# Optimization experiments

Hardware: AMD Instinct MI355X
Metric: run time of the kernel (lower is better)

Reference implementation:

```python
import jax, jax.numpy as jnp
import numpy as np

N_NODES = 100000
N_EDGES = 1200000
FEAT = 64
AVG_D_LOG = float(np.log(13.0))  # log(avg_degree + 1), avg_degree = 12
EPS_STD = 1e-5   # PNA std epsilon
EPS_BN = 1e-5    # torch BatchNorm1d default eps


def setup_inputs() -> dict:
    key = jax.random.key(0)
    k_h, k_norm, k_src, k_dst = jax.random.split(key, 4)
    h = jax.random.normal(k_h, (N_NODES, FEAT), dtype=jnp.float32)
    norm = jax.random.uniform(k_norm, (N_NODES, 1), dtype=jnp.float32)
    e = jnp.zeros((N_EDGES, 1), dtype=jnp.float32)  # unused by the layer
    src = jax.random.randint(k_src, (N_EDGES,), 0, N_NODES, dtype=jnp.int32)
    dst = jnp.sort(jax.random.randint(k_dst, (N_EDGES,), 0, N_NODES, dtype=jnp.int32))
    bn_weight = jnp.ones((FEAT,), dtype=jnp.float32)
    bn_bias = jnp.zeros((FEAT,), dtype=jnp.float32)
    return {"h": h, "norm": norm, "e": e, "bn_weight": bn_weight,
            "bn_bias": bn_bias, "src": src, "dst": dst}


def reference(h, norm, e, bn_weight, bn_bias, src, dst):
    N, F = h.shape
    hn = h * norm                           # [N, F] pre-scaled node features
    m = hn[src]                             # [E, F] gathered messages (copy_u)

    ones = jnp.ones_like(dst, dtype=hn.dtype)
    deg = jax.ops.segment_sum(ones, dst, num_segments=N, indices_are_sorted=True)  # [N]
    deg_safe = jnp.maximum(deg, 1.0)
    has_nb = (deg > 0)[:, None]             # zero in-degree nodes get zeros (DGL)

    s1 = jax.ops.segment_sum(m, dst, num_segments=N, indices_are_sorted=True)
    s2 = jax.ops.segment_sum(m * m, dst, num_segments=N, indices_are_sorted=True)
    mean = s1 / deg_safe[:, None]
    var = jax.nn.relu(s2 / deg_safe[:, None] - mean * mean)
    std = jnp.sqrt(var + EPS_STD)
    mx = jnp.where(has_nb, jax.ops.segment_max(m, dst, num_segments=N, indices_are_sorted=True), 0.0)
    mn = jnp.where(has_nb, jax.ops.segment_min(m, dst, num_segments=N, indices_are_sorted=True), 0.0)

    agg = jnp.concatenate([mean, mx, mn, std], axis=1)          # [N, 4F]

    logD = jnp.log(deg + 1.0)[:, None]                           # [N, 1]
    amp = agg * (logD / AVG_D_LOG)                               # amplification scaler
    att = agg * (AVG_D_LOG / jnp.where(logD > 0, logD, 1.0))     # attenuation scaler
    scaled = jnp.concatenate([agg, amp, att], axis=1)            # [N, 12F]
    scaled = jnp.where(has_nb, scaled, 0.0)

    out = jnp.concatenate([hn, scaled * norm], axis=1)           # [N, 13F]
    out = out.reshape(N, 13, F).mean(axis=1)                     # [N, F]
    out = jax.nn.relu(out)                                       # activation (dropout p=0)

    # BatchNorm1d, training mode (biased batch variance), affine
    mu = out.mean(axis=0)
    v = out.var(axis=0)
    out = (out - mu) / jnp.sqrt(v + EPS_BN) * bn_weight + bn_bias
    return out
```

## Files before the change

### kernel.cpp

```cpp
#include <hip/hip_runtime.h>
#include <hip/hip_fp16.h>
#include <math.h>
#include <float.h>

#define N_NODES 100000
#define N_EDGES 1200000
#define FEAT 64
#define AVG_D_LOG 2.5649493574615367f
#define EPS_STD 1e-5f
#define EPS_BN 1e-5
#define AGG_BLOCKS 12500
#define HN_BLOCKS 6250
#define SC_BLOCKS 4688
#define STAT1_BLOCKS 256
#define ROWS1 49

typedef _Float16 h2v __attribute__((ext_vector_type(2)));

#if __has_builtin(__builtin_fmaxf16)
#define H16MAX(a,b) __builtin_fmaxf16((a),(b))
#define H16MIN(a,b) __builtin_fminf16((a),(b))
#else
#define H16MAX(a,b) ((a) > (b) ? (a) : (b))
#define H16MIN(a,b) ((a) < (b) ? (a) : (b))
#endif

static __device__ __forceinline__ h2v h2vmax(h2v a, h2v b) {
#if __has_builtin(__builtin_elementwise_max)
    return __builtin_elementwise_max(a, b);
#else
    h2v r; r.x = H16MAX(a.x, b.x); r.y = H16MAX(a.y, b.y); return r;
#endif
}
static __device__ __forceinline__ h2v h2vmin(h2v a, h2v b) {
#if __has_builtin(__builtin_elementwise_min)
    return __builtin_elementwise_min(a, b);
#else
    h2v r; r.x = H16MIN(a.x, b.x); r.y = H16MIN(a.y, b.y); return r;
#endif
}
#if __has_builtin(__builtin_amdgcn_fdot2)
#define FDOT2(a,b,c) __builtin_amdgcn_fdot2((a),(b),(c),false)
#else
#define FDOT2(a,b,c) (__builtin_fmaf((float)(a).x,(float)(b).x, __builtin_fmaf((float)(a).y,(float)(b).y,(c))))
#endif

__global__ void __launch_bounds__(256) prep(
    const float* __restrict__ h, const float* __restrict__ norm,
    const int* __restrict__ dst,
    __half* __restrict__ hn_h, int* __restrict__ rowptr)
{
    const int b = blockIdx.x;
    if (b < HN_BLOCKS) {
        const size_t i4 = ((size_t)b * 256 + threadIdx.x) * 4;
        const int node = (int)(i4 >> 6);
        const float nr = norm[node];
        float4 v = *reinterpret_cast<const float4*>(h + i4);
        __half2 p0 = __floats2half2_rn(v.x * nr, v.y * nr);
        __half2 p1 = __floats2half2_rn(v.z * nr, v.w * nr);
        __half2* o = reinterpret_cast<__half2*>(hn_h + i4);
        o[0] = p0; o[1] = p1;
    } else {
        const int i = (b - HN_BLOCKS) * 256 + threadIdx.x;
        if (i >= N_EDGES) return;
        const int d1 = dst[i];
        const int d0 = (i == 0) ? -1 : dst[i - 1];
        for (int n = d0 + 1; n <= d1; ++n) rowptr[n] = i;
        if (i == N_EDGES - 1) {
            for (int n = d1 + 1; n <= N_NODES; ++n) rowptr[n] = N_EDGES;
        }
    }
}

template <bool OUT16>
__global__ void __launch_bounds__(256) pna_agg7(
    const __half* __restrict__ hn, const float* __restrict__ norm,
    const int* __restrict__ src, const int* __restrict__ rowptr,
    float* __restrict__ outf, __half* __restrict__ outh,
    float2* __restrict__ pstat)
{
    const int tid  = threadIdx.x;
    const int wid  = tid >> 6;
    const int lane = tid & 63;
    const int n0   = (blockIdx.x * 4 + wid) * 2;

    const int s0 = __builtin_amdgcn_readfirstlane(rowptr[n0]);
    const int e0 = __builtin_amdgcn_readfirstlane(rowptr[n0 + 1]);
    const int e1 = __builtin_amdgcn_readfirstlane(rowptr[n0 + 2]);
    const int degA = e0 - s0;
    const int degB = e1 - e0;

    const _Float16* __restrict__ hnf = (const _Float16*)hn;
    const float ownA = (float)hnf[(size_t)n0 * FEAT + lane];
    const float ownB = (float)hnf[(size_t)(n0 + 1) * FEAT + lane];

    float s1A = 0.f, s2A = 0.f, s1B = 0.f, s2B = 0.f;
    h2v mxA = { (_Float16)(-65504.f), (_Float16)(-65504.f) };
    h2v mnA = { (_Float16)( 65504.f), (_Float16)( 65504.f) };
    h2v mxB = mxA, mnB = mnA;
    const h2v ones = { (_Float16)1.f, (_Float16)1.f };

#define LOADP(J0,J1) ({ h2v w__;                                   \
        w__.x = hnf[(size_t)(J0) * FEAT + lane];                   \
        w__.y = hnf[(size_t)(J1) * FEAT + lane]; w__; })
#define ACCA(W) do { h2v w_ = (W);                                 \
        s1A = FDOT2(w_, ones, s1A); s2A = FDOT2(w_, w_, s2A);      \
        mxA = h2vmax(mxA, w_); mnA = h2vmin(mnA, w_); } while (0)
#define ACCB(W) do { h2v w_ = (W);                                 \
        s1B = FDOT2(w_, ones, s1B); s2B = FDOT2(w_, w_, s2B);      \
        mxB = h2vmax(mxB, w_); mnB = h2vmin(mnB, w_); } while (0)
#define ACCA1(W) do { _Float16 h_ = (W); float f_ = (float)h_;     \
        s1A += f_; s2A = __builtin_fmaf(f_, f_, s2A);              \
        mxA.x = H16MAX(mxA.x, h_); mnA.x = H16MIN(mnA.x, h_); } while (0)
#define ACCB1(W) do { _Float16 h_ = (W); float f_ = (float)h_;     \
        s1B += f_; s2B = __builtin_fmaf(f_, f_, s2B);              \
        mxB.x = H16MAX(mxB.x, h_); mnB.x = H16MIN(mnB.x, h_); } while (0)

    int ea = s0, eb = e0;
    while (ea + 8 <= e0 && eb + 8 <= e1) {
        const int a0 = src[ea+0], a1 = src[ea+1], a2 = src[ea+2], a3 = src[ea+3];
        const int a4 = src[ea+4], a5 = src[ea+5], a6 = src[ea+6], a7 = src[ea+7];
        const int b0 = src[eb+0], b1 = src[eb+1], b2 = src[eb+2], b3 = src[eb+3];
        const int b4 = src[eb+4], b5 = src[eb+5], b6 = src[eb+6], b7 = src[eb+7];
        h2v wa01 = LOADP(a0,a1), wa23 = LOADP(a2,a3), wa45 = LOADP(a4,a5), wa67 = LOADP(a6,a7);
        h2v wb01 = LOADP(b0,b1), wb23 = LOADP(b2,b3), wb45 = LOADP(b4,b5), wb67 = LOADP(b6,b7);
        ACCA(wa01); ACCA(wa23); ACCA(wa45); ACCA(wa67);
        ACCB(wb01); ACCB(wb23); ACCB(wb45); ACCB(wb67);
        ea += 8; eb += 8;
    }
    while (ea + 4 <= e0 && eb + 4 <= e1) {
        const int a0 = src[ea+0], a1 = src[ea+1], a2 = src[ea+2], a3 = src[ea+3];
        const int b0 = src[eb+0], b1 = src[eb+1], b2 = src[eb+2], b3 = src[eb+3];
        h2v wa01 = LOADP(a0,a1), wa23 = LOADP(a2,a3);
        h2v wb01 = LOADP(b0,b1), wb23 = LOADP(b2,b3);
        ACCA(wa01); ACCA(wa23);
        ACCB(wb01); ACCB(wb23);
        ea += 4; eb += 4;
    }
    for (; ea + 2 <= e0; ea += 2) {
        const int a0 = src[ea], a1 = src[ea+1];
        h2v w = LOADP(a0, a1);
        ACCA(w);
    }
    if (ea < e0) { ACCA1(hnf[(size_t)src[ea] * FEAT + lane]); }
    for (; eb + 2 <= e1; eb += 2) {
        const int b0 = src[eb], b1 = src[eb+1];
        h2v w = LOADP(b0, b1);
        ACCB(w);
    }
    if (eb < e1) { ACCB1(hnf[(size_t)src[eb] * FEAT + lane]); }
#undef LOADP
#undef ACCA
#undef ACCB
#undef ACCA1
#undef ACCB1

    float vA, vB;
    {
        float pre;
        if (degA > 0) {
            const float invd = 1.0f / (float)degA;
            const float mean = s1A * invd;
            const float var  = fmaxf(s2A * invd - mean * mean, 0.f);
            const float stdv = sqrtf(var + EPS_STD);
            const float mxf  = fmaxf((float)mxA.x, (float)mxA.y);
            const float mnf  = fminf((float)mnA.x, (float)mnA.y);
            const float logD = logf((float)degA + 1.0f);
            const float factor = norm[n0] * (1.0f + logD * (1.0f / AVG_D_LOG) + AVG_D_LOG / logD)
                                         * (1.0f / 13.0f);
            pre = ownA * (1.0f / 13.0f) + (mean + mxf + mnf + stdv) * factor;
        } else {
            pre = ownA * (1.0f / 13.0f);
        }
        vA = fmaxf(pre, 0.f);
    }
    {
        float pre;
        if (degB > 0) {
            const float invd = 1.0f / (float)degB;
            const float mean = s1B * invd;
            const float var  = fmaxf(s2B * invd - mean * mean, 0.f);
            const float stdv = sqrtf(var + EPS_STD);
            const float mxf  = fmaxf((float)mxB.x, (float)mxB.y);
            const float mnf  = fminf((float)mnB.x, (float)mnB.y);
            const float logD = logf((float)degB + 1.0f);
            const float factor = norm[n0 + 1] * (1.0f + logD * (1.0f / AVG_D_LOG) + AVG_D_LOG / logD)
                                             * (1.0f / 13.0f);
            pre = ownB * (1.0f / 13.0f) + (mean + mxf + mnf + stdv) * factor;
        } else {
            pre = ownB * (1.0f / 13.0f);
        }
        vB = fmaxf(pre, 0.f);
    }

    if (OUT16) {
        outh[(size_t)n0 * FEAT + lane]       = __float2half_rn(vA);
        outh[(size_t)(n0 + 1) * FEAT + lane] = __float2half_rn(vB);
    } else {
        outf[(size_t)n0 * FEAT + lane]       = vA;
        outf[(size_t)(n0 + 1) * FEAT + lane] = vB;
    }

    {
        __shared__ float lsS[4][64];
        __shared__ float lsQ[4][64];
        lsS[wid][lane] = vA + vB;
        lsQ[wid][lane] = vA * vA + vB * vB;
        __syncthreads();
        if (tid < 64) {
            float2 p;
            p.x = lsS[0][tid] + lsS[1][tid] + lsS[2][tid] + lsS[3][tid];
            p.y = lsQ[0][tid] + lsQ[1][tid] + lsQ[2][tid] + lsQ[3][tid];
            pstat[(size_t)blockIdx.x * 64 + tid] = p;
        }
    }
}

__global__ void __launch_bounds__(256) bn_stats1(
    const float2* __restrict__ pstat, float2* __restrict__ partial)
{
    const int tid  = threadIdx.x;
    const int w    = tid >> 6;
    const int lane = tid & 63;
    const int r0 = (int)blockIdx.x * ROWS1;
    const int r1 = min(r0 + ROWS1, AGG_BLOCKS);
    float S = 0.f, Q = 0.f;
    for (int r = r0 + w; r < r1; r += 4) {
        float2 p = pstat[(size_t)r * 64 + lane];
        S += p.x; Q += p.y;
    }
    __shared__ float sS[4][64], sQ[4][64];
    sS[w][lane] = S; sQ[w][lane] = Q;
    __syncthreads();
    if (tid < 64) {
        float2 o;
        o.x = sS[0][tid] + sS[1][tid] + sS[2][tid] + sS[3][tid];
        o.y = sQ[0][tid] + sQ[1][tid] + sQ[2][tid] + sQ[3][tid];
        partial[(size_t)blockIdx.x * 64 + tid] = o;
    }
}

__global__ void __launch_bounds__(256) bn_stats2(
    const float2* __restrict__ partial,
    const float* __restrict__ w, const float* __restrict__ b,
    float2* __restrict__ ss)
{
    const int tid = threadIdx.x;
    const int g   = tid >> 6;
    const int f   = tid & 63;
    double S = 0.0, Q = 0.0;
    for (int blk = g; blk < STAT1_BLOCKS; blk += 4) {
        float2 p = partial[(size_t)blk * 64 + f];
        S += (double)p.x; Q += (double)p.y;
    }
    __shared__ double dS[4][64], dQ[4][64];
    dS[g][f] = S; dQ[g][f] = Q;
    __syncthreads();
    if (tid < 64) {
        double s = dS[0][tid] + dS[1][tid] + dS[2][tid] + dS[3][tid];
        double q = dQ[0][tid] + dQ[1][tid] + dQ[2][tid] + dQ[3][tid];
        double mu   = s / (double)N_NODES;
        double var  = q / (double)N_NODES - mu * mu;
        double rstd = 1.0 / sqrt(var + EPS_BN);
        float sc = (float)rstd * w[tid];
        float2 o; o.x = sc; o.y = b[tid] - (float)mu * sc;
        ss[tid] = o;
    }
}

__global__ void __launch_bounds__(256) bn_apply3(
    const __half* __restrict__ out1h, float* __restrict__ out,
    const float2* __restrict__ ss)
{
    __shared__ float sS[64], sH[64];
    if (threadIdx.x < 64) {
        float2 p = ss[threadIdx.x];
        sS[threadIdx.x] = p.x; sH[threadIdx.x] = p.y;
    }
    __syncthreads();
    const size_t i4 = ((size_t)blockIdx.x * 256 + threadIdx.x) * 4;
    const __half2* ip = reinterpret_cast<const __half2*>(out1h + i4);
    __half2 a = ip[0], b = ip[1];
    const int f = (int)(i4 & 63);
    float4 v;
    v.x = __low2float(a)  * sS[f + 0] + sH[f + 0];
    v.y = __high2float(a) * sS[f + 1] + sH[f + 1];
    v.z = __low2float(b)  * sS[f + 2] + sH[f + 2];
    v.w = __high2float(b) * sS[f + 3] + sH[f + 3];
    *reinterpret_cast<float4*>(out + i4) = v;
}

__global__ void __launch_bounds__(256) bn_apply2(
    float* __restrict__ out, const float2* __restrict__ ss)
{
    __shared__ float sS[64], sH[64];
    if (threadIdx.x < 64) {
        float2 p = ss[threadIdx.x];
        sS[threadIdx.x] = p.x; sH[threadIdx.x] = p.y;
    }
    __syncthreads();
    const size_t i4 = ((size_t)blockIdx.x * 256 + threadIdx.x) * 4;
    float4 v = *reinterpret_cast<const float4*>(out + i4);
    const int f = (int)(i4 & 63);
    v.x = v.x * sS[f + 0] + sH[f + 0];
    v.y = v.y * sS[f + 1] + sH[f + 1];
    v.z = v.z * sS[f + 2] + sH[f + 2];
    v.w = v.w * sS[f + 3] + sH[f + 3];
    *reinterpret_cast<float4*>(out + i4) = v;
}

extern "C" void kernel_launch(void* const* d_in, const int* in_sizes, int n_in,
                              void* d_out, int out_size, void* d_ws, size_t ws_size,
                              hipStream_t stream) {
    const float* h    = (const float*)d_in[0];
    const float* norm = (const float*)d_in[1];
    const float* bnw  = (const float*)d_in[3];
    const float* bnb  = (const float*)d_in[4];
    const int*   src  = (const int*)d_in[5];
    const int*   dst  = (const int*)d_in[6];
    float* out = (float*)d_out;

    char* ws = (char*)d_ws;
    size_t o = 0;
    __half* hnbuf = (__half*)(ws + o);
    o += (((size_t)N_NODES * FEAT * sizeof(__half)) + 255) & ~(size_t)255;
    int* rowptr = (int*)(ws + o);
    o += (((size_t)(N_NODES + 1) * sizeof(int)) + 255) & ~(size_t)255;
    float2* ss = (float2*)(ws + o); o += 512;
    float2* partial = (float2*)(ws + o);
    o += (size_t)STAT1_BLOCKS * 64 * sizeof(float2);
    float2* pstat = (float2*)(ws + o);
    o += (size_t)AGG_BLOCKS * 64 * sizeof(float2);
    const size_t need_mid = o;
    __half* out1h = (__half*)(ws + o);
    const size_t need_fast = o + (size_t)N_NODES * FEAT * sizeof(__half);

    prep<<<HN_BLOCKS + SC_BLOCKS, 256, 0, stream>>>(h, norm, dst, hnbuf, rowptr);

    if (ws_size >= need_fast) {
        pna_agg7<true><<<AGG_BLOCKS, 256, 0, stream>>>(hnbuf, norm, src, rowptr,
                                                       nullptr, out1h, pstat);
        bn_stats1<<<STAT1_BLOCKS, 256, 0, stream>>>(pstat, partial);
        bn_stats2<<<1, 256, 0, stream>>>(partial, bnw, bnb, ss);
        bn_apply3<<<HN_BLOCKS, 256, 0, stream>>>(out1h, out, ss);
    } else if (ws_size >= need_mid) {
        pna_agg7<false><<<AGG_BLOCKS, 256, 0, stream>>>(hnbuf, norm, src, rowptr,
                                                        out, nullptr, pstat);
        bn_stats1<<<STAT1_BLOCKS, 256, 0, stream>>>(pstat, partial);
        bn_stats2<<<1, 256, 0, stream>>>(partial, bnw, bnb, ss);
        bn_apply2<<<HN_BLOCKS, 256, 0, stream>>>(out, ss);
    }
}
```

Measured before the change: 82.98 us.

## Use degree lookup table, fp16 partial stats, and single-pass BN stats kernel

Precomputes 1/deg and the combined PNA scaler factor for degrees below 256 in an extra prep block, replacing per-node log and divide in the aggregation kernel with a table load. Stores per-block BatchNorm partial sums as half2 instead of float2, halving that traffic. Replaces the two-stage stats reduction with one 64-block kernel in which each block reduces one feature. The fp16 partial sums of squares risk precision loss or overflow, and the per-feature reads in the new kernel are strided.

New measurement: 77.16 us. -7.0%, faster.

```diff
diff --git a/kernel.cpp b/kernel.cpp
--- a/kernel.cpp
+++ b/kernel.cpp
@@ -6,14 +6,13 @@
 #define N_NODES 100000
 #define N_EDGES 1200000
 #define FEAT 64
-#define AVG_D_LOG 2.5649493574615367f
+#define AVG_D_LOG 2.5649493574615367
 #define EPS_STD 1e-5f
 #define EPS_BN 1e-5
 #define AGG_BLOCKS 12500
 #define HN_BLOCKS 6250
 #define SC_BLOCKS 4688
-#define STAT1_BLOCKS 256
-#define ROWS1 49
+#define TAB_N 256
 
 typedef _Float16 h2v __attribute__((ext_vector_type(2)));
 
@@ -48,7 +47,8 @@
 __global__ void __launch_bounds__(256) prep(
     const float* __restrict__ h, const float* __restrict__ norm,
     const int* __restrict__ dst,
-    __half* __restrict__ hn_h, int* __restrict__ rowptr)
+    __half* __restrict__ hn_h, int* __restrict__ rowptr,
+    float2* __restrict__ tab)
 {
     const int b = blockIdx.x;
     if (b < HN_BLOCKS) {
@@ -60,7 +60,7 @@
         __half2 p1 = __floats2half2_rn(v.z * nr, v.w * nr);
         __half2* o = reinterpret_cast<__half2*>(hn_h + i4);
         o[0] = p0; o[1] = p1;
-    } else {
+    } else if (b < HN_BLOCKS + SC_BLOCKS) {
         const int i = (b - HN_BLOCKS) * 256 + threadIdx.x;
         if (i >= N_EDGES) return;
         const int d1 = dst[i];
@@ -69,15 +69,26 @@
         if (i == N_EDGES - 1) {
             for (int n = d1 + 1; n <= N_NODES; ++n) rowptr[n] = N_EDGES;
         }
+    } else {
+        const int d = threadIdx.x;
+        double invd = (d > 0) ? 1.0 / (double)d : 1.0;
+        double fb = 0.0;
+        if (d > 0) {
+            double lg = log((double)d + 1.0);
+            fb = (1.0 + lg / AVG_D_LOG + AVG_D_LOG / lg) / 13.0;
+        }
+        float2 t; t.x = (float)invd; t.y = (float)fb;
+        tab[d] = t;
     }
 }
 
 template <bool OUT16>
-__global__ void __launch_bounds__(256) pna_agg7(
+__global__ void __launch_bounds__(256) pna_agg8(
     const __half* __restrict__ hn, const float* __restrict__ norm,
     const int* __restrict__ src, const int* __restrict__ rowptr,
+    const float2* __restrict__ tab,
     float* __restrict__ outf, __half* __restrict__ outh,
-    float2* __restrict__ pstat)
+    __half2* __restrict__ pstat)
 {
     const int tid  = threadIdx.x;
     const int wid  = tid >> 6;
@@ -159,15 +170,19 @@
     {
         float pre;
         if (degA > 0) {
-            const float invd = 1.0f / (float)degA;
+            float invd, fb;
+            if (degA < TAB_N) { float2 t = tab[degA]; invd = t.x; fb = t.y; }
+            else {
+                invd = 1.0f / (float)degA;
+                float lg = logf((float)degA + 1.0f);
+                fb = (1.0f + lg * (float)(1.0 / AVG_D_LOG) + (float)AVG_D_LOG / lg) * (1.0f / 13.0f);
+            }
             const float mean = s1A * invd;
             const float var  = fmaxf(s2A * invd - mean * mean, 0.f);
             const float stdv = sqrtf(var + EPS_STD);
             const float mxf  = fmaxf((float)mxA.x, (float)mxA.y);
             const float mnf  = fminf((float)mnA.x, (float)mnA.y);
-            const float logD = logf((float)degA + 1.0f);
-            const float factor = norm[n0] * (1.0f + logD * (1.0f / AVG_D_LOG) + AVG_D_LOG / logD)
-                                         * (1.0f / 13.0f);
+            const float factor = norm[n0] * fb;
             pre = ownA * (1.0f / 13.0f) + (mean + mxf + mnf + stdv) * factor;
         } else {
             pre = ownA * (1.0f / 13.0f);
@@ -177,15 +192,19 @@
     {
         float pre;
         if (degB > 0) {
-            const float invd = 1.0f / (float)degB;
+            float invd, fb;
+            if (degB < TAB_N) { float2 t = tab[degB]; invd = t.x; fb = t.y; }
+            else {
+                invd = 1.0f / (float)degB;
+                float lg = logf((float)degB + 1.0f);
+                fb = (1.0f + lg * (float)(1.0 / AVG_D_LOG) + (float)AVG_D_LOG / lg) * (1.0f / 13.0f);
+            }
             const float mean = s1B * invd;
             const float var  = fmaxf(s2B * invd - mean * mean, 0.f);
             const float stdv = sqrtf(var + EPS_STD);
             const float mxf  = fmaxf((float)mxB.x, (float)mxB.y);
             const float mnf  = fminf((float)mnB.x, (float)mnB.y);
-            const float logD = logf((float)degB + 1.0f);
-            const float factor = norm[n0 + 1] * (1.0f + logD * (1.0f / AVG_D_LOG) + AVG_D_LOG / logD)
-                                             * (1.0f / 13.0f);
+            const float factor = norm[n0 + 1] * fb;
             pre = ownB * (1.0f / 13.0f) + (mean + mxf + mnf + stdv) * factor;
         } else {
             pre = ownB * (1.0f / 13.0f);
@@ -208,63 +227,39 @@
         lsQ[wid][lane] = vA * vA + vB * vB;
         __syncthreads();
         if (tid < 64) {
-            float2 p;
-            p.x = lsS[0][tid] + lsS[1][tid] + lsS[2][tid] + lsS[3][tid];
-            p.y = lsQ[0][tid] + lsQ[1][tid] + lsQ[2][tid] + lsQ[3][tid];
-            pstat[(size_t)blockIdx.x * 64 + tid] = p;
-        }
-    }
-}
-
-__global__ void __launch_bounds__(256) bn_stats1(
-    const float2* __restrict__ pstat, float2* __restrict__ partial)
-{
-    const int tid  = threadIdx.x;
-    const int w    = tid >> 6;
-    const int lane = tid & 63;
-    const int r0 = (int)blockIdx.x * ROWS1;
-    const int r1 = min(r0 + ROWS1, AGG_BLOCKS);
-    float S = 0.f, Q = 0.f;
-    for (int r = r0 + w; r < r1; r += 4) {
-        float2 p = pstat[(size_t)r * 64 + lane];
-        S += p.x; Q += p.y;
-    }
-    __shared__ float sS[4][64], sQ[4][64];
-    sS[w][lane] = S; sQ[w][lane] = Q;
-    __syncthreads();
-    if (tid < 64) {
-        float2 o;
-        o.x = sS[0][tid] + sS[1][tid] + sS[2][tid] + sS[3][tid];
-        o.y = sQ[0][tid] + sQ[1][tid] + sQ[2][tid] + sQ[3][tid];
-        partial[(size_t)blockIdx.x * 64 + tid] = o;
-    }
-}
-
-__global__ void __launch_bounds__(256) bn_stats2(
-    const float2* __restrict__ partial,
+            float S = lsS[0][tid] + lsS[1][tid] + lsS[2][tid] + lsS[3][tid];
+            float Q = lsQ[0][tid] + lsQ[1][tid] + lsQ[2][tid] + lsQ[3][tid];
+            pstat[(size_t)blockIdx.x * 64 + tid] = __floats2half2_rn(S, Q);
+        }
+    }
+}
+
+__global__ void __launch_bounds__(256) bn_statsM(
+    const __half2* __restrict__ pstat,
     const float* __restrict__ w, const float* __restrict__ b,
     float2* __restrict__ ss)
 {
+    const int f   = (int)blockIdx.x;
     const int tid = threadIdx.x;
-    const int g   = tid >> 6;
-    const int f   = tid & 63;
-    double S = 0.0, Q = 0.0;
-    for (int blk = g; blk < STAT1_BLOCKS; blk += 4) {
-        float2 p = partial[(size_t)blk * 64 + f];
-        S += (double)p.x; Q += (double)p.y;
-    }
-    __shared__ double dS[4][64], dQ[4][64];
-    dS[g][f] = S; dQ[g][f] = Q;
+    float S = 0.f, Q = 0.f;
+    for (int i = tid; i < AGG_BLOCKS; i += 256) {
+        __half2 p = pstat[(size_t)i * 64 + f];
+        S += __low2float(p); Q += __high2float(p);
+    }
+    __shared__ double rs[256], rq[256];
+    rs[tid] = (double)S; rq[tid] = (double)Q;
     __syncthreads();
-    if (tid < 64) {
-        double s = dS[0][tid] + dS[1][tid] + dS[2][tid] + dS[3][tid];
-        double q = dQ[0][tid] + dQ[1][tid] + dQ[2][tid] + dQ[3][tid];
-        double mu   = s / (double)N_NODES;
-        double var  = q / (double)N_NODES - mu * mu;
+    for (int s = 128; s > 0; s >>= 1) {
+        if (tid < s) { rs[tid] += rs[tid + s]; rq[tid] += rq[tid + s]; }
+        __syncthreads();
+    }
+    if (tid == 0) {
+        double mu   = rs[0] / (double)N_NODES;
+        double var  = rq[0] / (double)N_NODES - mu * mu;
         double rstd = 1.0 / sqrt(var + EPS_BN);
-        float sc = (float)rstd * w[tid];
-        float2 o; o.x = sc; o.y = b[tid] - (float)mu * sc;
-        ss[tid] = o;
+        float sc = (float)rstd * w[f];
+        float2 o; o.x = sc; o.y = b[f] - (float)mu * sc;
+        ss[f] = o;
     }
 }
 
@@ -327,27 +322,24 @@
     int* rowptr = (int*)(ws + o);
     o += (((size_t)(N_NODES + 1) * sizeof(int)) + 255) & ~(size_t)255;
     float2* ss = (float2*)(ws + o); o += 512;
-    float2* partial = (float2*)(ws + o);
-    o += (size_t)STAT1_BLOCKS * 64 * sizeof(float2);
-    float2* pstat = (float2*)(ws + o);
-    o += (size_t)AGG_BLOCKS * 64 * sizeof(float2);
+    float2* tab = (float2*)(ws + o); o += (size_t)TAB_N * sizeof(float2);
+    __half2* pstat = (__half2*)(ws + o);
+    o += (size_t)AGG_BLOCKS * 64 * sizeof(__half2);
     const size_t need_mid = o;
     __half* out1h = (__half*)(ws + o);
     const size_t need_fast = o + (size_t)N_NODES * FEAT * sizeof(__half);
 
-    prep<<<HN_BLOCKS + SC_BLOCKS, 256, 0, stream>>>(h, norm, dst, hnbuf, rowptr);
+    prep<<<HN_BLOCKS + SC_BLOCKS + 1, 256, 0, stream>>>(h, norm, dst, hnbuf, rowptr, tab);
 
     if (ws_size >= need_fast) {
-        pna_agg7<true><<<AGG_BLOCKS, 256, 0, stream>>>(hnbuf, norm, src, rowptr,
+        pna_agg8<true><<<AGG_BLOCKS, 256, 0, stream>>>(hnbuf, norm, src, rowptr, tab,
                                                        nullptr, out1h, pstat);
-        bn_stats1<<<STAT1_BLOCKS, 256, 0, stream>>>(pstat, partial);
-        bn_stats2<<<1, 256, 0, stream>>>(partial, bnw, bnb, ss);
+        bn_statsM<<<64, 256, 0, stream>>>(pstat, bnw, bnb, ss);
         bn_apply3<<<HN_BLOCKS, 256, 0, stream>>>(out1h, out, ss);
     } else if (ws_size >= need_mid) {
-        pna_agg7<false><<<AGG_BLOCKS, 256, 0, stream>>>(hnbuf, norm, src, rowptr,
+        pna_agg8<false><<<AGG_BLOCKS, 256, 0, stream>>>(hnbuf, norm, src, rowptr, tab,
                                                         out, nullptr, pstat);
-        bn_stats1<<<STAT1_BLOCKS, 256, 0, stream>>>(pstat, partial);
-        bn_stats2<<<1, 256, 0, stream>>>(partial, bnw, bnb, ss);
+        bn_statsM<<<64, 256, 0, stream>>>(pstat, bnw, bnb, ss);
         bn_apply2<<<HN_BLOCKS, 256, 0, stream>>>(out, ss);
     }
 }
```
